# Performance work log

Measured on AMD Instinct MI355X. Metric: run time of the kernel, lower is better.

## Reference

```python
import jax, jax.numpy as jnp
import numpy as np

H, DH, C = 16, 64, 1024  # num_head, head_size, embed_size
B, T = 4, 2048

def setup_inputs() -> dict:
    key = jax.random.key(0)
    ks = jax.random.split(key, 6)
    s = 1.0 / np.sqrt(C)
    x  = jax.random.normal(ks[0], (B, T, C), dtype=jnp.float32)
    # per-head projection weights, stacked: [H, C, DH] (PyTorch Linear computes x @ W.T; we store W.T directly)
    Wq = jax.random.uniform(ks[1], (H, C, DH), dtype=jnp.float32, minval=-s, maxval=s)
    Wk = jax.random.uniform(ks[2], (H, C, DH), dtype=jnp.float32, minval=-s, maxval=s)
    Wv = jax.random.uniform(ks[3], (H, C, DH), dtype=jnp.float32, minval=-s, maxval=s)
    Wo = jax.random.uniform(ks[4], (C, C), dtype=jnp.float32, minval=-s, maxval=s)
    bo = jax.random.uniform(ks[5], (C,), dtype=jnp.float32, minval=-s, maxval=s)
    return {"x": x, "Wq": Wq, "Wk": Wk, "Wv": Wv, "Wo": Wo, "bo": bo}

def reference(x, Wq, Wk, Wv, Wo, bo):
    # Dropout layers act as identity (eval mode).
    q = jnp.einsum('btc,hcd->bhtd', x, Wq)
    k = jnp.einsum('btc,hcd->bhtd', x, Wk)
    v = jnp.einsum('btc,hcd->bhtd', x, Wv)
    scale = 1.0 / np.sqrt(DH).astype(np.float32)
    wei = jnp.einsum('bhtd,bhsd->bhts', q, k) * scale  # [B,H,T,T]
    Tn = x.shape[1]
    causal = jnp.tril(jnp.ones((Tn, Tn), dtype=bool))
    wei = jnp.where(causal, wei, -jnp.inf)
    wei = jax.nn.softmax(wei, axis=-1)
    out = jnp.einsum('bhts,bhsd->bhtd', wei, v)  # [B,H,T,DH]
    out = out.transpose(0, 2, 1, 3).reshape(x.shape[0], Tn, H * DH)  # concat heads
    return out @ Wo + bo
```

## Files before the change

kernel.cpp:

```cpp
#include <hip/hip_runtime.h>
#include <hip/hip_bf16.h>

typedef __attribute__((ext_vector_type(8))) short short8;
typedef __attribute__((ext_vector_type(4))) float floatx4;
typedef __attribute__((ext_vector_type(4))) unsigned int u32x4;

static constexpr int Hn = 16, DHn = 64, Cn = 1024;
static constexpr int Bn = 4, Tn = 2048;
static constexpr int Mtot = Bn * Tn;
static constexpr size_t QKV_STRIDE = (size_t)Bn * Hn * Tn * DHn;

__device__ __forceinline__ unsigned short bfbits(float f) {
    __hip_bfloat16 h = __float2bfloat16(f);
    return __builtin_bit_cast(unsigned short, h);
}

__device__ __forceinline__ unsigned int cvtpk(float a, float b) {
    unsigned int r;
    asm("v_cvt_pk_bf16_f32 %0, %1, %2" : "=v"(r) : "v"(a), "v"(b));
    return r;
}

__device__ __forceinline__ void gl_lds16(const void* g, void* lds_base) {
    __builtin_amdgcn_global_load_lds(
        (const __attribute__((address_space(1))) unsigned int*)g,
        (__attribute__((address_space(3))) unsigned int*)lds_base, 16, 0, 0);
}

__global__ void conv_kernel(const float4* __restrict__ src, ushort4* __restrict__ dst, int n4) {
    int i = blockIdx.x * blockDim.x + threadIdx.x;
    if (i < n4) {
        float4 v = src[i];
        ushort4 o;
        o.x = bfbits(v.x); o.y = bfbits(v.y); o.z = bfbits(v.z); o.w = bfbits(v.w);
        dst[i] = o;
    }
}

__global__ void tconv3_kernel(const float* __restrict__ Wq, const float* __restrict__ Wk,
                              const float* __restrict__ Wv, __hip_bfloat16* __restrict__ wT) {
    __shared__ float tile[32][33];
    const int z = blockIdx.z, w = z >> 4, hh = z & 15;
    const float* s = (w == 0 ? Wq : (w == 1 ? Wk : Wv)) + (size_t)hh * Cn * DHn;
    __hip_bfloat16* d = wT + (size_t)z * Cn * DHn;
    const float scale = (w == 0) ? 0.125f * 1.44269504088896f : 1.0f;
    int c0 = blockIdx.x * 32;
    int r0 = blockIdx.y * 32;
    int tx = threadIdx.x, ty = threadIdx.y;
    for (int i = 0; i < 4; ++i) {
        int r = r0 + ty + i * 8;
        tile[ty + i * 8][tx] = s[(size_t)r * DHn + c0 + tx];
    }
    __syncthreads();
    for (int i = 0; i < 4; ++i) {
        int c = c0 + ty + i * 8;
        d[(size_t)c * Cn + r0 + tx] = __float2bfloat16(tile[tx][ty + i * 8] * scale);
    }
}

__global__ void tconv_kernel(const float* __restrict__ src, __hip_bfloat16* __restrict__ dst,
                             int R, int C) {
    __shared__ float tile[32][33];
    int c0 = blockIdx.x * 32;
    int r0 = blockIdx.y * 32;
    int tx = threadIdx.x, ty = threadIdx.y;
    for (int i = 0; i < 4; ++i) {
        int r = r0 + ty + i * 8;
        tile[ty + i * 8][tx] = src[(size_t)r * C + c0 + tx];
    }
    __syncthreads();
    for (int i = 0; i < 4; ++i) {
        int c = c0 + ty + i * 8;
        dst[(size_t)c * R + r0 + tx] = __float2bfloat16(tile[tx][ty + i * 8]);
    }
}

template<int MODE>
__global__ __launch_bounds__(256) void gemm_kernel(
    const __hip_bfloat16* __restrict__ A,
    const __hip_bfloat16* __restrict__ BT,
    const float* __restrict__ bias,
    __hip_bfloat16* __restrict__ out_qkv,
    float* __restrict__ out_f32)
{
    constexpr int K = Cn;
    constexpr int NSTEP = K / 64;
    __shared__ char smem[65536];

    const int m0 = blockIdx.x * 128;
    const int n0 = blockIdx.y * 128;

    const int tid = threadIdx.x;
    const int lane = tid & 63, wid = tid >> 6;
    const int wy = wid >> 1, wx = wid & 1;
    const int fr = lane & 15, g = lane >> 4;
    const int rxor = (fr & 7) << 4;

    floatx4 acc[4][4] = {};

    int srow[4], scol[4], doff[4];
#pragma unroll
    for (int i = 0; i < 4; ++i) {
        int byteoff = wid * 4096 + i * 1024 + lane * 16;
        int r = byteoff >> 7;
        int ch = (byteoff >> 4) & 7;
        srow[i] = r;
        scol[i] = (ch ^ (r & 7)) << 3;
        doff[i] = wid * 4096 + i * 1024;
    }

#pragma unroll
    for (int i = 0; i < 4; ++i) {
        gl_lds16(&A[(size_t)(m0 + srow[i]) * K + scol[i]], smem + doff[i]);
        gl_lds16(&BT[(size_t)(n0 + srow[i]) * K + scol[i]], smem + 16384 + doff[i]);
    }
    asm volatile("s_waitcnt vmcnt(0)" ::: "memory");
    asm volatile("s_barrier" ::: "memory");

    int cur = 0;
    for (int t = 0; t < NSTEP; ++t) {
        if (t + 1 < NSTEP) {
            const int k0 = (t + 1) * 64;
            char* dst = smem + (cur ^ 1) * 32768;
#pragma unroll
            for (int i = 0; i < 4; ++i) {
                gl_lds16(&A[(size_t)(m0 + srow[i]) * K + k0 + scol[i]], dst + doff[i]);
                gl_lds16(&BT[(size_t)(n0 + srow[i]) * K + k0 + scol[i]], dst + 16384 + doff[i]);
            }
        }
        const char* lA0 = smem + cur * 32768;
        const char* lB0 = lA0 + 16384;
#pragma unroll
        for (int kk = 0; kk < 2; ++kk) {
            short8 af[4], bf[4];
#pragma unroll
            for (int t4 = 0; t4 < 4; ++t4) {
                af[t4] = *(const short8*)(lA0 + (wy * 64 + t4 * 16 + fr) * 128 + ((kk * 64 + g * 16) ^ rxor));
                bf[t4] = *(const short8*)(lB0 + (wx * 64 + t4 * 16 + fr) * 128 + ((kk * 64 + g * 16) ^ rxor));
            }
            __builtin_amdgcn_s_setprio(1);
#pragma unroll
            for (int tm = 0; tm < 4; ++tm)
#pragma unroll
                for (int tn = 0; tn < 4; ++tn)
                    acc[tm][tn] = __builtin_amdgcn_mfma_f32_16x16x32_bf16(af[tm], bf[tn], acc[tm][tn], 0, 0, 0);
            __builtin_amdgcn_s_setprio(0);
        }
        asm volatile("s_waitcnt vmcnt(0)" ::: "memory");
        asm volatile("s_barrier" ::: "memory");
        cur ^= 1;
    }

    for (int tm = 0; tm < 4; ++tm) {
        int rbase = m0 + wy * 64 + tm * 16 + g * 4;
        for (int tn = 0; tn < 4; ++tn) {
            int nc = n0 + wx * 64 + tn * 16 + fr;
            if (MODE == 0) {
                int w = nc >> 10, rem = nc & 1023, hh = rem >> 6, dd = rem & 63;
                if (w == 2) {
                    int b = rbase >> 11, t0 = rbase & 2047;
                    int pos = (t0 & ~31) | (((t0 >> 2) & 3) << 3) | (((t0 >> 4) & 1) << 2);
                    ushort4 pk;
                    pk.x = bfbits(acc[tm][tn][0]);
                    pk.y = bfbits(acc[tm][tn][1]);
                    pk.z = bfbits(acc[tm][tn][2]);
                    pk.w = bfbits(acc[tm][tn][3]);
                    *(ushort4*)(&out_qkv[2 * QKV_STRIDE +
                        ((size_t)((b * Hn + hh) * DHn + dd)) * Tn + pos]) = pk;
                } else {
                    for (int r = 0; r < 4; ++r) {
                        int m = rbase + r;
                        int b = m >> 11, t = m & 2047;
                        out_qkv[(size_t)w * QKV_STRIDE + (((size_t)(b * Hn + hh) * Tn + t) << 6) + dd] =
                            __float2bfloat16(acc[tm][tn][r]);
                    }
                }
            } else {
                float bs = bias[nc];
                for (int r = 0; r < 4; ++r) {
                    int m = rbase + r;
                    out_f32[(size_t)m * Cn + nc] = acc[tm][tn][r] + bs;
                }
            }
        }
    }
}

__global__ __launch_bounds__(256, 4) void attn_kernel(
    const __hip_bfloat16* __restrict__ q,
    const __hip_bfloat16* __restrict__ k,
    const __hip_bfloat16* __restrict__ vt,
    __hip_bfloat16* __restrict__ ao)
{
    __shared__ char smem[32768];

    const int id = blockIdx.x;
    const int xcd = id & 7;
    const int rnk = id >> 3;
    const int tile = 15 - (rnk >> 3);
    const int bh = xcd * 8 + (rnk & 7);
    const int b = bh >> 4, h = bh & 15;
    const int tid = threadIdx.x, lane = tid & 63, wid = tid >> 6;
    const int fr = lane & 15, g = lane >> 4;
    const size_t base = (size_t)bh * Tn * DHn;
    const int rxor = (fr & 7) << 4;

    const int r0 = wid * 16 + (lane >> 3);
    const int c8 = ((lane & 7) ^ (r0 & 7)) * 8;
    const int ldk0 = wid * 2048;

    short8 ones;
#pragma unroll
    for (int z = 0; z < 8; ++z) ones[z] = (short)0x3F80;

    const int qb0 = tile * 128;
    const int q0 = qb0 + wid * 32;
    const int nkv = qb0 / 64 + 2;

    short8 aq[2][2];
#pragma unroll
    for (int rq = 0; rq < 2; ++rq)
#pragma unroll
        for (int kk = 0; kk < 2; ++kk)
            aq[rq][kk] = *(const short8*)(&q[base + (size_t)(q0 + rq * 16 + fr) * DHn + kk * 32 + g * 8]);

    floatx4 o[2][4] = {};
    floatx4 o5[2] = {};

    {
        char* kd = smem + ldk0;
        char* vd = smem + 16384 + ldk0;
        gl_lds16(&k[base + (size_t)r0 * DHn + c8], kd);
        gl_lds16(&k[base + (size_t)(r0 + 8) * DHn + c8], kd + 1024);
        gl_lds16(&vt[base + (size_t)r0 * Tn + c8], vd);
        gl_lds16(&vt[base + (size_t)(r0 + 8) * Tn + c8], vd + 1024);
    }
    asm volatile("s_waitcnt vmcnt(0)" ::: "memory");
    __builtin_amdgcn_s_barrier();

    int cur = 0;
    for (int j = 0; j < nkv; ++j) {
        const int kv0 = j * 64;

        {
            const int nv0 = kv0 + 64;
            char* kd = smem + (cur ^ 1) * 8192 + ldk0;
            char* vd = smem + 16384 + (cur ^ 1) * 8192 + ldk0;
            gl_lds16(&k[base + (size_t)(nv0 + r0) * DHn + c8], kd);
            gl_lds16(&k[base + (size_t)(nv0 + r0 + 8) * DHn + c8], kd + 1024);
            gl_lds16(&vt[base + (size_t)r0 * Tn + nv0 + c8], vd);
            gl_lds16(&vt[base + (size_t)(r0 + 8) * Tn + nv0 + c8], vd + 1024);
        }

        if (kv0 < q0 + 32) {
            const char* lkc = smem + cur * 8192;
            const char* lvc = smem + 16384 + cur * 8192;

            floatx4 s[2][4] = {};
            __builtin_amdgcn_s_setprio(1);
#pragma unroll
            for (int kk = 0; kk < 2; ++kk)
#pragma unroll
                for (int cg = 0; cg < 4; ++cg) {
                    short8 kf = *(const short8*)(lkc + (cg * 16 + fr) * 128 + ((g * 16 + kk * 64) ^ rxor));
                    s[0][cg] = __builtin_amdgcn_mfma_f32_16x16x32_bf16(kf, aq[0][kk], s[0][cg], 0, 0, 0);
                    s[1][cg] = __builtin_amdgcn_mfma_f32_16x16x32_bf16(kf, aq[1][kk], s[1][cg], 0, 0, 0);
                }
            __builtin_amdgcn_s_setprio(0);

            if (kv0 + 64 > q0) {
#pragma unroll
                for (int rq = 0; rq < 2; ++rq) {
                    int qg = q0 + rq * 16 + fr;
#pragma unroll
                    for (int cg = 0; cg < 4; ++cg) {
                        int kg = kv0 + cg * 16 + g * 4;
#pragma unroll
                        for (int r = 0; r < 4; ++r)
                            if (kg + r > qg) s[rq][cg][r] = -1e30f;
                    }
                }
            }

            short8 pb[2][2];
#pragma unroll
            for (int rq = 0; rq < 2; ++rq) {
#pragma unroll
                for (int cg = 0; cg < 4; ++cg)
#pragma unroll
                    for (int r = 0; r < 4; ++r)
                        s[rq][cg][r] = __builtin_amdgcn_exp2f(s[rq][cg][r]);
#pragma unroll
                for (int kt = 0; kt < 2; ++kt) {
                    u32x4 wv;
                    wv[0] = cvtpk(s[rq][2 * kt][0],     s[rq][2 * kt][1]);
                    wv[1] = cvtpk(s[rq][2 * kt][2],     s[rq][2 * kt][3]);
                    wv[2] = cvtpk(s[rq][2 * kt + 1][0], s[rq][2 * kt + 1][1]);
                    wv[3] = cvtpk(s[rq][2 * kt + 1][2], s[rq][2 * kt + 1][3]);
                    pb[rq][kt] = __builtin_bit_cast(short8, wv);
                }
            }

            __builtin_amdgcn_s_setprio(1);
#pragma unroll
            for (int rq = 0; rq < 2; ++rq)
#pragma unroll
                for (int kt = 0; kt < 2; ++kt)
                    o5[rq] = __builtin_amdgcn_mfma_f32_16x16x32_bf16(ones, pb[rq][kt], o5[rq], 0, 0, 0);
#pragma unroll
            for (int kt = 0; kt < 2; ++kt)
#pragma unroll
                for (int dg = 0; dg < 4; ++dg) {
                    const int vrow = (dg * 16 + fr) * 128;
                    short8 vf = *(const short8*)(lvc + vrow + ((kt * 64 + g * 16) ^ rxor));
                    o[0][dg] = __builtin_amdgcn_mfma_f32_16x16x32_bf16(vf, pb[0][kt], o[0][dg], 0, 0, 0);
                    o[1][dg] = __builtin_amdgcn_mfma_f32_16x16x32_bf16(vf, pb[1][kt], o[1][dg], 0, 0, 0);
                }
            __builtin_amdgcn_s_setprio(0);
        }

        asm volatile("s_waitcnt vmcnt(0)" ::: "memory");
        __builtin_amdgcn_s_barrier();
        cur ^= 1;
    }

    char* myscr = smem + wid * 4096;
    const int rr = lane >> 2, cc = lane & 3;
#pragma unroll
    for (int rq = 0; rq < 2; ++rq) {
        const float inv = 1.0f / o5[rq][0];
#pragma unroll
        for (int dg = 0; dg < 4; ++dg) {
            floatx4 wv = o[rq][dg] * inv;
            *(floatx4*)(myscr + fr * 256 + ((dg * 64 + g * 16) ^ rxor)) = wv;
        }
        asm volatile("s_waitcnt lgkmcnt(0)" ::: "memory");
        float4 f0 = *(const float4*)(myscr + rr * 256 + ((cc * 64 + 0) ^ ((rr & 7) << 4)));
        float4 f1 = *(const float4*)(myscr + rr * 256 + ((cc * 64 + 16) ^ ((rr & 7) << 4)));
        float4 f2 = *(const float4*)(myscr + rr * 256 + ((cc * 64 + 32) ^ ((rr & 7) << 4)));
        float4 f3 = *(const float4*)(myscr + rr * 256 + ((cc * 64 + 48) ^ ((rr & 7) << 4)));
        short8 pk0, pk1;
        pk0[0] = (short)bfbits(f0.x); pk0[1] = (short)bfbits(f0.y);
        pk0[2] = (short)bfbits(f0.z); pk0[3] = (short)bfbits(f0.w);
        pk0[4] = (short)bfbits(f1.x); pk0[5] = (short)bfbits(f1.y);
        pk0[6] = (short)bfbits(f1.z); pk0[7] = (short)bfbits(f1.w);
        pk1[0] = (short)bfbits(f2.x); pk1[1] = (short)bfbits(f2.y);
        pk1[2] = (short)bfbits(f2.z); pk1[3] = (short)bfbits(f2.w);
        pk1[4] = (short)bfbits(f3.x); pk1[5] = (short)bfbits(f3.y);
        pk1[6] = (short)bfbits(f3.z); pk1[7] = (short)bfbits(f3.w);
        size_t orow = ((size_t)(b * Tn + q0 + rq * 16 + rr)) * Cn + h * 64 + cc * 16;
        *(short8*)(&ao[orow]) = pk0;
        *(short8*)(&ao[orow + 8]) = pk1;
        asm volatile("s_waitcnt lgkmcnt(0)" ::: "memory");
    }
}

extern "C" void kernel_launch(void* const* d_in, const int* in_sizes, int n_in,
                              void* d_out, int out_size, void* d_ws, size_t ws_size,
                              hipStream_t stream) {
    const float* x  = (const float*)d_in[0];
    const float* Wq = (const float*)d_in[1];
    const float* Wk = (const float*)d_in[2];
    const float* Wv = (const float*)d_in[3];
    const float* Wo = (const float*)d_in[4];
    const float* bo = (const float*)d_in[5];
    float* out = (float*)d_out;

    char* ws = (char*)d_ws;
    __hip_bfloat16* xb  = (__hip_bfloat16*)(ws);
    __hip_bfloat16* wT  = (__hip_bfloat16*)(ws + 16777216);
    __hip_bfloat16* woT = (__hip_bfloat16*)(ws + 23068672);
    __hip_bfloat16* qb  = (__hip_bfloat16*)(ws + 25165824);
    __hip_bfloat16* ao  = (__hip_bfloat16*)(ws + 75497472);

    conv_kernel<<<(Mtot * Cn / 4 + 255) / 256, 256, 0, stream>>>(
        (const float4*)x, (ushort4*)xb, Mtot * Cn / 4);
    tconv3_kernel<<<dim3(2, 32, 48), dim3(32, 8), 0, stream>>>(Wq, Wk, Wv, wT);
    tconv_kernel<<<dim3(32, 32, 1), dim3(32, 8), 0, stream>>>(Wo, woT, Cn, Cn);

    gemm_kernel<0><<<dim3(Mtot / 128, 3072 / 128), 256, 0, stream>>>(
        xb, wT, nullptr, qb, nullptr);

    attn_kernel<<<dim3(1024), 256, 0, stream>>>(
        qb, qb + QKV_STRIDE, qb + 2 * QKV_STRIDE, ao);

    gemm_kernel<1><<<dim3(Mtot / 128, Cn / 128), 256, 0, stream>>>(
        ao, woT, bo, nullptr, out);
}
```

Before: 138.5 us.

## Deepen GEMM prefetch to two tiles ahead with register-staged fragments

Restructures the GEMM main loop so global-to-LDS loads run two K-tiles ahead instead of one, waiting only on the older batch with vmcnt(8). Each step reads all fragments for the tile into registers, waits for LDS reads and barriers, then reuses the freed buffer for the next prefetch before issuing the MFMAs. This is meant to hide global memory latency behind more compute. In exchange it adds an extra barrier per step, doubles the fragment registers held, and issues redundant clamped loads at the tail.

```diff
diff --git a/kernel.cpp b/kernel.cpp
--- a/kernel.cpp
+++ b/kernel.cpp
@@ -109,47 +109,51 @@
         doff[i] = wid * 4096 + i * 1024;
     }
 
-#pragma unroll
-    for (int i = 0; i < 4; ++i) {
-        gl_lds16(&A[(size_t)(m0 + srow[i]) * K + scol[i]], smem + doff[i]);
-        gl_lds16(&BT[(size_t)(n0 + srow[i]) * K + scol[i]], smem + 16384 + doff[i]);
-    }
-    asm volatile("s_waitcnt vmcnt(0)" ::: "memory");
-    asm volatile("s_barrier" ::: "memory");
-
-    int cur = 0;
+#define STAGE_T(tile, buf)                                                              \
+    {                                                                                   \
+        const int k0s = (tile) * 64;                                                    \
+        char* dstb = smem + (buf) * 32768;                                              \
+        _Pragma("unroll")                                                               \
+        for (int i = 0; i < 4; ++i) {                                                   \
+            gl_lds16(&A[(size_t)(m0 + srow[i]) * K + k0s + scol[i]], dstb + doff[i]);   \
+            gl_lds16(&BT[(size_t)(n0 + srow[i]) * K + k0s + scol[i]], dstb + 16384 + doff[i]); \
+        }                                                                               \
+    }
+
+    STAGE_T(0, 0);
+    STAGE_T(1, 1);
+
     for (int t = 0; t < NSTEP; ++t) {
-        if (t + 1 < NSTEP) {
-            const int k0 = (t + 1) * 64;
-            char* dst = smem + (cur ^ 1) * 32768;
-#pragma unroll
-            for (int i = 0; i < 4; ++i) {
-                gl_lds16(&A[(size_t)(m0 + srow[i]) * K + k0 + scol[i]], dst + doff[i]);
-                gl_lds16(&BT[(size_t)(n0 + srow[i]) * K + k0 + scol[i]], dst + 16384 + doff[i]);
+        asm volatile("s_waitcnt vmcnt(8)" ::: "memory");
+        __builtin_amdgcn_s_barrier();
+
+        const char* lA0 = smem + (t & 1) * 32768;
+        const char* lB0 = lA0 + 16384;
+        short8 af[2][4], bf[2][4];
+#pragma unroll
+        for (int kk = 0; kk < 2; ++kk)
+#pragma unroll
+            for (int t4 = 0; t4 < 4; ++t4) {
+                af[kk][t4] = *(const short8*)(lA0 + (wy * 64 + t4 * 16 + fr) * 128 + ((kk * 64 + g * 16) ^ rxor));
+                bf[kk][t4] = *(const short8*)(lB0 + (wx * 64 + t4 * 16 + fr) * 128 + ((kk * 64 + g * 16) ^ rxor));
             }
-        }
-        const char* lA0 = smem + cur * 32768;
-        const char* lB0 = lA0 + 16384;
-#pragma unroll
-        for (int kk = 0; kk < 2; ++kk) {
-            short8 af[4], bf[4];
-#pragma unroll
-            for (int t4 = 0; t4 < 4; ++t4) {
-                af[t4] = *(const short8*)(lA0 + (wy * 64 + t4 * 16 + fr) * 128 + ((kk * 64 + g * 16) ^ rxor));
-                bf[t4] = *(const short8*)(lB0 + (wx * 64 + t4 * 16 + fr) * 128 + ((kk * 64 + g * 16) ^ rxor));
-            }
-            __builtin_amdgcn_s_setprio(1);
+        asm volatile("s_waitcnt lgkmcnt(0)" ::: "memory");
+        __builtin_amdgcn_s_barrier();
+
+        int nt = t + 2; if (nt > NSTEP - 1) nt = NSTEP - 1;
+        STAGE_T(nt, t & 1);
+
+        __builtin_amdgcn_s_setprio(1);
+#pragma unroll
+        for (int kk = 0; kk < 2; ++kk)
 #pragma unroll
             for (int tm = 0; tm < 4; ++tm)
 #pragma unroll
                 for (int tn = 0; tn < 4; ++tn)
-                    acc[tm][tn] = __builtin_amdgcn_mfma_f32_16x16x32_bf16(af[tm], bf[tn], acc[tm][tn], 0, 0, 0);
-            __builtin_amdgcn_s_setprio(0);
-        }
-        asm volatile("s_waitcnt vmcnt(0)" ::: "memory");
-        asm volatile("s_barrier" ::: "memory");
-        cur ^= 1;
-    }
+                    acc[tm][tn] = __builtin_amdgcn_mfma_f32_16x16x32_bf16(af[kk][tm], bf[kk][tn], acc[tm][tn], 0, 0, 0);
+        __builtin_amdgcn_s_setprio(0);
+    }
+#undef STAGE_T
 
     for (int tm = 0; tm < 4; ++tm) {
         int rbase = m0 + wy * 64 + tm * 16 + g * 4;
```

After: 146.8 us. 6.0% more time.
